# Kernel tuning notes

Measured on AMD Instinct MI355X. Metric: run time of the kernel, lower is better.

## Reference

```python
import jax, jax.numpy as jnp
import numpy as np

Lx = 32
Ly = 32
L = Lx * Ly          # 1024 lattice sites
N_E = L              # occupied orbitals (half filling of 2L BdG states)
HOPPING_LIST = (0, 2)
SWAVE_LIST = (0,)
DWAVE_LIST = (0,)


def _circulant_from_flat(flat, pad_front):
    """Faithful vectorized form of unroll_vpot_Mat: vmat[i,j] = V((xj-xi)%Lx,(yj-yi)%Ly)."""
    zero = jnp.zeros((1,), flat.dtype)
    v = jnp.concatenate([zero, flat, zero]) if pad_front else jnp.concatenate([flat, zero])
    A = v.reshape(1 + Lx // 2, 1 + Ly // 2)
    comp = jnp.block([[A, jnp.fliplr(A[:, 1:-1])],
                      [jnp.flipud(A[1:-1, :]), jnp.flipud(jnp.fliplr(A[1:-1, 1:-1]))]])  # (Lx,Ly)
    idx = jnp.arange(L)
    xs, ys = idx // Ly, idx % Ly
    DX = (xs[None, :] - xs[:, None]) % Lx
    DY = (ys[None, :] - ys[:, None]) % Ly
    return comp[DX, DY]  # (L, L)


def _fill_NN(X, nbr_a, nbr_b, sign):
    """Vectorized fill_NN_X/Y_matrix: scatter (X[j]-X[i])*sign[i,j] at (i, j=nbr)."""
    i = jnp.arange(L)
    M = jnp.zeros((L, L), X.dtype)
    M = M.at[i, nbr_a].set((X[nbr_a] - X[i]) * sign[i, nbr_a])
    M = M.at[i, nbr_b].set((X[nbr_b] - X[i]) * sign[i, nbr_b])
    return M


def setup_inputs() -> dict:
    rng = np.random.default_rng(0)
    key = jax.random.key(0)
    ks = jax.random.split(key, 16)

    # periodic square-lattice neighbor table: dirs 0:+y 1:+x 2:-y 3:-x
    idx = np.arange(L)
    x, y = idx // Ly, idx % Ly
    ivic = np.stack([
        x * Ly + (y + 1) % Ly,
        ((x + 1) % Lx) * Ly + y,
        x * Ly + (y - 1) % Ly,
        ((x - 1) % Lx) * Ly + y,
    ], axis=1)[:, :, None].astype(np.int32)  # (L,4,1)

    sign_b = (2.0 * rng.integers(0, 2, size=(L, L)) - 1.0).astype(np.float32)
    stagg = ((-1.0) ** (x + y)).astype(np.float32)

    def sym(k, n_mat):
        R = jax.random.normal(k, (n_mat, 2 * L, 2 * L), dtype=jnp.float32) * 0.05
        return 0.5 * (R + jnp.swapaxes(R, -1, -2))

    nJ = (1 + Lx // 2) * (1 + Ly // 2) - 1  # 288
    occupied = rng.permutation(2 * L)[:N_E].astype(np.int32)

    return {
        "occupied_sites": jnp.asarray(occupied),
        "xloc": jnp.asarray(rng.integers(0, 2 * L, size=(L,)).astype(np.int32)),
        "S_z": jnp.asarray((2.0 * rng.integers(0, 2, size=(L,)) - 1.0).astype(np.float32)),
        "X_Phonons": jax.random.normal(ks[0], (L,), dtype=jnp.float32) * 0.1,
        "Y_Phonons": jax.random.normal(ks[1], (L,), dtype=jnp.float32) * 0.1,
        "hopping_values": jnp.full((len(HOPPING_LIST),), -1.0, dtype=jnp.float32),
        "sWave_pair_values": jnp.full((len(SWAVE_LIST),), 0.1, dtype=jnp.float32),
        "dWave_pair_values": jnp.full((len(DWAVE_LIST),), 0.1, dtype=jnp.float32),
        "Jastrow_spin": jax.random.normal(ks[2], (nJ,), dtype=jnp.float32) * 0.01,
        "Jastrow_coupling_Xel": jax.random.normal(ks[3], (nJ - 1,), dtype=jnp.float32) * 0.01,
        "Jastrow_coupling_Yel": jax.random.normal(ks[4], (nJ - 1,), dtype=jnp.float32) * 0.01,
        "phonons_XX_jastrow": jax.random.normal(ks[5], (nJ,), dtype=jnp.float32) * 0.01,
        "phonons_XY_jastrow": jax.random.normal(ks[6], (nJ,), dtype=jnp.float32) * 0.01,
        "phonons_YY_jastrow": jax.random.normal(ks[7], (nJ,), dtype=jnp.float32) * 0.01,
        "g": jnp.array([0.7], dtype=jnp.float32),
        "f_Swave": jnp.array([0.05], dtype=jnp.float32),
        "f_dwave": jnp.array([0.05], dtype=jnp.float32),
        "z_x": jnp.array([0.5], dtype=jnp.float32),
        "z_y": jnp.array([0.5], dtype=jnp.float32),
        "x_rescaled": jnp.array([0.3], dtype=jnp.float32),
        "y_rescaled": jnp.array([0.3], dtype=jnp.float32),
        "hopping_array_matrices": sym(ks[8], 3),
        "sWave_pair_array_matrices": sym(ks[9], 1),
        "dWave_pair_array_matrices": sym(ks[10], 1),
        "ivic": jnp.asarray(ivic),
        "bond_hopping_difference_sign": jnp.asarray(sign_b),
        "stagg_x": jnp.asarray(stagg),
        "stagg_y": jnp.asarray(stagg),
    }


def reference(occupied_sites, xloc, S_z, X_Phonons, Y_Phonons,
              hopping_values, sWave_pair_values, dWave_pair_values,
              Jastrow_spin, Jastrow_coupling_Xel, Jastrow_coupling_Yel,
              phonons_XX_jastrow, phonons_XY_jastrow, phonons_YY_jastrow,
              g, f_Swave, f_dwave, z_x, z_y, x_rescaled, y_rescaled,
              hopping_array_matrices, sWave_pair_array_matrices, dWave_pair_array_matrices,
              ivic, bond_hopping_difference_sign, stagg_x, stagg_y):
    sign_b = bond_hopping_difference_sign

    H0 = -1.0 * hopping_array_matrices[1]
    H0 = H0 + jnp.einsum('i,ijk->jk', hopping_values, hopping_array_matrices[jnp.array(HOPPING_LIST)])
    H0 = H0 + jnp.einsum('i,ijk->jk', sWave_pair_values, sWave_pair_array_matrices[jnp.array(SWAVE_LIST)])
    H0 = H0 + jnp.einsum('i,ijk->jk', dWave_pair_values, dWave_pair_array_matrices[jnp.array(DWAVE_LIST)])

    phonX = _fill_NN(X_Phonons, ivic[:, 1, 0], ivic[:, 3, 0], sign_b)
    phonY = _fill_NN(Y_Phonons, ivic[:, 0, 0], ivic[:, 2, 0], sign_b)
    P = phonX + phonY
    M = phonX - phonY
    Z = jnp.zeros((L, L), H0.dtype)
    H0 = H0 + g[0] * jnp.block([[P, Z], [Z, -P]])
    H0 = H0 + f_Swave[0] * jnp.block([[Z, P], [P, Z]])
    H0 = H0 + f_dwave[0] * jnp.block([[Z, M], [M, Z]])

    eigs, U = jnp.linalg.eigh(H0)
    sgn, logdet = jnp.linalg.slogdet(U[occupied_sites, :N_E])

    vmat = _circulant_from_flat(Jastrow_spin, pad_front=False)
    log_jastrow = S_z @ vmat @ S_z

    coh = -0.5 * x_rescaled[0] * jnp.sum((X_Phonons - z_x * stagg_x) ** 2)
    coh = coh - 0.5 * y_rescaled[0] * jnp.sum((Y_Phonons - z_y * stagg_y) ** 2)
    vXX = _circulant_from_flat(phonons_XX_jastrow, pad_front=False)
    vXY = _circulant_from_flat(phonons_XY_jastrow, pad_front=False)
    vYY = _circulant_from_flat(phonons_YY_jastrow, pad_front=False)
    coh = coh + X_Phonons @ vXX @ X_Phonons
    coh = coh + Y_Phonons @ vXY @ X_Phonons + X_Phonons @ vXY @ Y_Phonons
    coh = coh + Y_Phonons @ vYY @ Y_Phonons

    # el-phonon jastrows: vmat * (X[i]-X[j]) * sign[i,j]
    vXel = _circulant_from_flat(Jastrow_coupling_Xel, pad_front=True) \
        * (X_Phonons[:, None] - X_Phonons[None, :]) * sign_b
    vYel = _circulant_from_flat(Jastrow_coupling_Yel, pad_front=True) \
        * (Y_Phonons[:, None] - Y_Phonons[None, :]) * sign_b
    coh = coh + S_z @ vXel @ S_z + S_z @ vYel @ S_z

    return logdet + coh + log_jastrow
```

## Files before the change

### kernel.cpp

```cpp
#include <hip/hip_runtime.h>
#include <math.h>

#define NN 2048
#define LL 1024
#define NSWB 5
#define NROUNDS (NSWB * 63)
#define PITER 10
#define JTAU 1e-6f
#define STREAK_FULL 2016


typedef float vf4 __attribute__((ext_vector_type(4)));

__global__ void build_H(const float* __restrict__ hop,  const float* __restrict__ swm,
                        const float* __restrict__ dwm,  const float* __restrict__ hv,
                        const float* __restrict__ sv,   const float* __restrict__ dv,
                        const float* __restrict__ X,    const float* __restrict__ Y,
                        const int*   __restrict__ ivic, const float* __restrict__ sb,
                        const float* __restrict__ gg,   const float* __restrict__ fS,
                        const float* __restrict__ fd,   float* __restrict__ W)
{
    int idx = blockIdx.x * 256 + threadIdx.x;
    int r = idx >> 11, c = idx & (NN - 1);
    float hv0 = hv[0], hv1 = hv[1], sv0 = sv[0], dv0 = dv[0];
    float g0 = gg[0], fS0 = fS[0], fd0 = fd[0];

    float val = 0.f;
    #pragma unroll
    for (int t = 0; t < 2; ++t) {
        int rr = t ? c : r;
        int cc = t ? r : c;
        int e  = rr * NN + cc;
        float v = hv0 * hop[e] - hop[NN*NN + e] + hv1 * hop[2*NN*NN + e]
                + sv0 * swm[e] + dv0 * dwm[e];
        int i = rr & (LL - 1), j = cc & (LL - 1);
        float px = 0.f, py = 0.f;
        float s = sb[i * LL + j];
        int n0 = ivic[i*4+0], n1 = ivic[i*4+1], n2 = ivic[i*4+2], n3 = ivic[i*4+3];
        if (j == n1 || j == n3) px = (X[j] - X[i]) * s;
        if (j == n0 || j == n2) py = (Y[j] - Y[i]) * s;
        float P = px + py, Mm = px - py;
        bool rlo = rr < LL, clo = cc < LL;
        if (rlo && clo)        v += g0 * P;
        else if (!rlo && !clo) v -= g0 * P;
        else                   v += fS0 * P + fd0 * Mm;
        val += 0.5f * v;
    }
    W[idx] = val;
}

__global__ void powv_init(float* v)
{
    int i = blockIdx.x * 256 + threadIdx.x;
    if (i < NN) {
        unsigned h = (unsigned)i * 2654435761u;
        h ^= h >> 13; h *= 2246822519u; h ^= h >> 16;
        v[i] = ((h >> 8) * (1.0f / 16777216.f)) - 0.5f;
    }
}

__global__ void matvec(const float* __restrict__ W, const float* __restrict__ vin,
                       float* __restrict__ vout, double* accslot)
{
    __shared__ float red[256];
    int row = blockIdx.x, tid = threadIdx.x;
    const float* wr = W + (size_t)row * NN;
    float s = 0.f;
    for (int j = tid; j < NN; j += 256) s += wr[j] * vin[j];
    red[tid] = s; __syncthreads();
    for (int off = 128; off; off >>= 1) { if (tid < off) red[tid] += red[tid + off]; __syncthreads(); }
    if (tid == 0) { float y = red[0]; vout[row] = y; atomicAdd(accslot, (double)y * (double)y); }
}

__global__ void add_shift(float* W, const double* acc)
{
    int i = blockIdx.x * 256 + threadIdx.x;
    if (i < NN) {
        double n1 = acc[8 + PITER - 1], n0 = acc[8 + PITER - 2];
        float rho = (float)sqrt(n1 / (n0 > 0.0 ? n0 : 1.0));
        W[(size_t)i * NN + i] += 1.45f * rho;
    }
}

__device__ __forceinline__ void pair_groups(int pair, int r, int& gp, int& gq)
{
    if (pair == 0) gp = 0;
    else { int t1 = pair - 1 + r; if (t1 >= 63) t1 -= 63; gp = 1 + t1; }
    int t2 = 62 - pair + r; if (t2 >= 63) t2 -= 63; gq = 1 + t2;
}

__device__ __forceinline__ int  ald(const int* p)
{ return __hip_atomic_load(p, __ATOMIC_RELAXED, __HIP_MEMORY_SCOPE_AGENT); }
__device__ __forceinline__ void ast(int* p, int v)
{ __hip_atomic_store(p, v, __ATOMIC_RELAXED, __HIP_MEMORY_SCOPE_AGENT); }
__device__ __forceinline__ void afst(float* p, float v)
{ __hip_atomic_store(p, v, __ATOMIC_RELAXED, __HIP_MEMORY_SCOPE_AGENT); }
__device__ __forceinline__ void afadd(float* p, float v)
{ (void)__hip_atomic_fetch_add(p, v, __ATOMIC_RELAXED, __HIP_MEMORY_SCOPE_AGENT); }

__device__ __forceinline__ vf4 cld4(const float* p)
{ vf4 d; asm volatile("global_load_dwordx4 %0, %1, off sc0 sc1" : "=v"(d) : "v"(p)); return d; }
__device__ __forceinline__ void cst4(float* p, vf4 v)
{ asm volatile("global_store_dwordx4 %0, %1, off sc0 sc1" :: "v"(p), "v"(v) : "memory"); }
__device__ __forceinline__ void cst1(float* p, float v)
{ asm volatile("global_store_dword %0, %1, off sc0 sc1" :: "v"(p), "v"(v) : "memory"); }
__device__ __forceinline__ void waitvm0()
{ asm volatile("s_waitcnt vmcnt(0)" ::: "memory"); __builtin_amdgcn_sched_barrier(0); }

__device__ __forceinline__ void gridbar(int* bars, int phase)
{
    waitvm0();
    __syncthreads();
    if (threadIdx.x == 0) {
        int g = blockIdx.x & 7;
        int old = __hip_atomic_fetch_add(&bars[g * 1024], 1,
                      __ATOMIC_RELAXED, __HIP_MEMORY_SCOPE_AGENT);
        if (old == phase * 64 - 1) {
            int t = __hip_atomic_fetch_add(&bars[8 * 1024], 1,
                        __ATOMIC_RELAXED, __HIP_MEMORY_SCOPE_AGENT);
            if (t == phase * 8 - 1)
                ast(&bars[9 * 1024], phase);
        }
        while (ald(&bars[9 * 1024]) < phase)
            __builtin_amdgcn_s_sleep(8);
        asm volatile("" ::: "memory");
    }
    __syncthreads();
}

__global__ __launch_bounds__(512, 4) void jac_fused(float* __restrict__ W,
                                                    float* __restrict__ Sg,
                                                    float* __restrict__ Vbuf,
                                                    int* __restrict__ gctl,
                                                    int* __restrict__ bars,
                                                    int* __restrict__ pbars,
                                                    int* __restrict__ vstat)
{
    __shared__ float TT[64][132];
    __shared__ float S[64][65];
    __shared__ float Vs[64][64];
    __shared__ float csC[32], csS[32];
    __shared__ int   pk[32], qk[32];
    __shared__ int   active;
    __shared__ int   nact[2];

    const int tid    = threadIdx.x;
    const int bid    = blockIdx.x;
    const int gpair  = bid >> 4, chunk = bid & 15;
    const int r0     = chunk * 128;
    const bool issol = (chunk == (gpair >> 1));
    const bool ldr   = (issol && tid == 0);
    int gphase = 0, pphase = 0;

    for (int rr = 0; rr < NROUNDS; ++rr) {
        int r = rr; while (r >= 63) r -= 63;
        int gp, gq; pair_groups(gpair, r, gp, gq);
        int c1 = ald(&gctl[2 + gp]);
        int c2 = ald(&gctl[2 + gq]);
        bool hint = (c1 >= 63 && c2 >= 63);
        if (!hint) ++pphase;

        {
            float* bufn = Sg + ((size_t)(((rr + 1) & 1) * 32 + gpair)) * 4096 + chunk * 256;
            if (tid < 256) afst(&bufn[tid], 0.f);
        }

        if (!hint) {
            {
                int q  = tid & 31, r4 = q << 2;
                int cA = tid >> 5;
                vf4 t0 = cld4(W + (size_t)(gp * 32 + cA     ) * NN + r0 + r4);
                vf4 t1 = cld4(W + (size_t)(gp * 32 + cA + 16) * NN + r0 + r4);
                vf4 t2 = cld4(W + (size_t)(gq * 32 + cA     ) * NN + r0 + r4);
                vf4 t3 = cld4(W + (size_t)(gq * 32 + cA + 16) * NN + r0 + r4);
                waitvm0();
                *(vf4*)&TT[cA     ][r4] = t0;
                *(vf4*)&TT[cA + 16][r4] = t1;
                *(vf4*)&TT[cA + 32][r4] = t2;
                *(vf4*)&TT[cA + 48][r4] = t3;
            }
            __syncthreads();
            int tr = tid & 15, tc = tid >> 4;
            float acc[4][2] = {};
            for (int r4 = 0; r4 < 128; r4 += 4) {
                float a[4][4], b[2][4];
                #pragma unroll
                for (int m = 0; m < 4; ++m) *(float4*)a[m] = *(const float4*)&TT[tr + 16*m][r4];
                #pragma unroll
                for (int n = 0; n < 2; ++n) *(float4*)b[n] = *(const float4*)&TT[tc + 32*n][r4];
                #pragma unroll
                for (int m = 0; m < 4; ++m)
                    #pragma unroll
                    for (int n = 0; n < 2; ++n)
                        #pragma unroll
                        for (int k = 0; k < 4; ++k)
                            acc[m][n] += a[m][k] * b[n][k];
            }
            float* bufc = Sg + ((size_t)((rr & 1) * 32 + gpair)) * 4096;
            #pragma unroll
            for (int m = 0; m < 4; ++m)
                #pragma unroll
                for (int n = 0; n < 2; ++n)
                    afadd(&bufc[(tr + 16*m) * 64 + (tc + 32*n)], acc[m][n]);
            waitvm0();
            __syncthreads();
            if (tid == 0)
                (void)__hip_atomic_fetch_add(&pbars[gpair * 1024], 1,
                          __ATOMIC_RELAXED, __HIP_MEMORY_SCOPE_AGENT);
        }

        int do_apply = 0;
        if (hint) {
            if (ldr) {
                ast(&gctl[2 + gp], c1 + 1);
                ast(&gctl[2 + gq], c2 + 1);
                int old = __hip_atomic_fetch_add(&gctl[1], 1,
                              __ATOMIC_RELAXED, __HIP_MEMORY_SCOPE_AGENT);
                if (old + 1 >= STREAK_FULL) ast(&gctl[0], 1);
            }
        } else if (issol) {
            if (tid == 0) {
                while (ald(&pbars[gpair * 1024]) < 16 * pphase)
                    __builtin_amdgcn_s_sleep(4);
                active = 0;
            }
            if (tid < 2) nact[tid] = 0;
            __syncthreads();
            {
                const float* bufc = Sg + ((size_t)((rr & 1) * 32 + gpair)) * 4096;
                vf4 s0 = cld4(bufc + 4 * tid);
                vf4 s1 = cld4(bufc + 4 * (tid + 512));
                waitvm0();
                int i0 = tid >> 4, j0 = (tid & 15) << 2;
                int i1 = (tid + 512) >> 4;
                S[i0][j0] = s0.x; S[i0][j0+1] = s0.y; S[i0][j0+2] = s0.z; S[i0][j0+3] = s0.w;
                S[i1][j0] = s1.x; S[i1][j0+1] = s1.y; S[i1][j0+2] = s1.z; S[i1][j0+3] = s1.w;
            }
            __syncthreads();
            int loc = 0;
            for (int e = tid; e < 4096; e += 512) {
                int i = e >> 6, j = e & 63;
                if (i < j) {
                    float o = S[i][j];
                    if (o * o > JTAU * S[i][i] * S[j][j]) loc = 1;
                }
            }
            if (loc) active = 1;
            __syncthreads();
            if (!active) {
                if (tid == 0) {
                    ast(&gctl[2 + gp], c1 + 1);
                    ast(&gctl[2 + gq], c2 + 1);
                    int old = __hip_atomic_fetch_add(&gctl[1], 1,
                                  __ATOMIC_RELAXED, __HIP_MEMORY_SCOPE_AGENT);
                    if (old + 1 >= STREAK_FULL) ast(&gctl[0], 1);
                    ast(&vstat[gpair * 32], pphase * 2);
                }
            } else {
                do_apply = 1;
                if (tid == 0) {
                    ast(&gctl[2 + gp], 0);
                    ast(&gctl[2 + gq], 0);
                    __hip_atomic_exchange(&gctl[1], 0,
                        __ATOMIC_RELAXED, __HIP_MEMORY_SCOPE_AGENT);
                }
                int lane = tid & 63, wv = tid >> 6;
                float v[8];
                #pragma unroll
                for (int i = 0; i < 8; ++i) v[i] = (8 * wv + i == lane) ? 1.f : 0.f;

                for (int r2 = 0; r2 < 63; ++r2) {
                    if (tid < 32) {
                        int k = tid, p, q;
                        if (k == 0) p = 0;
                        else { int t1 = k - 1 + r2; if (t1 >= 63) t1 -= 63; p = 1 + t1; }
                        int t2 = 62 - k + r2; if (t2 >= 63) t2 -= 63; q = 1 + t2;
                        float app = S[p][p], aqq = S[q][q], apq = S[p][q];
                        float c = 1.f, s = 0.f;
                        if (apq * apq > JTAU * app * aqq) {
                            float tau = (aqq - app) * __builtin_amdgcn_rcpf(2.f * apq);
                            float sq  = __builtin_amdgcn_sqrtf(fmaf(tau, tau, 1.f));
                            float t   = (tau >= 0.f ? 1.f : -1.f) *
                                        __builtin_amdgcn_rcpf(fabsf(tau) + sq);
                            c = __builtin_amdgcn_rsqf(fmaf(t, t, 1.f));
                            s = t * c;
                            nact[r2 & 1] = 1;
                        }
                        csC[k] = c; csS[k] = s; pk[k] = p; qk[k] = q;
                    }
                    if (tid == 256) nact[(r2 + 1) & 1] = 0;
                    __syncthreads();
                    if (!nact[r2 & 1]) break;
                    for (int u = tid; u < 1024; u += 512) {
                        int ki = u >> 5, kj = u & 31;
                        float si_ = csS[ki], sj_ = csS[kj];
                        if (si_ == 0.f && sj_ == 0.f) continue;
                        float ci_ = csC[ki], cj_ = csC[kj];
                        int pi = pk[ki], qi = qk[ki], pj = pk[kj], qj = qk[kj];
                        float a  = S[pi][pj], b  = S[pi][qj];
                        float c2 = S[qi][pj], d  = S[qi][qj];
                        float a1 = cj_ * a  - sj_ * b,  b1 = sj_ * a  + cj_ * b;
                        float c1 = cj_ * c2 - sj_ * d,  d1 = sj_ * c2 + cj_ * d;
                        S[pi][pj] = ci_ * a1 - si_ * c1;
                        S[qi][pj] = si_ * a1 + ci_ * c1;
                        S[pi][qj] = ci_ * b1 - si_ * d1;
                        S[qi][qj] = si_ * b1 + ci_ * d1;
                    }
                    {
                        int k;
                        if (lane == 0) k = 0;
                        else { int t = lane - 1 - r2; if (t < 0) t += 63;
                               k = (t <= 30) ? (t + 1) : (62 - t); }
                        float s_ = csS[k];
                        if (s_ != 0.f) {
                            float c_ = csC[k];
                            int p = pk[k], q = qk[k];
                            bool isp = (lane == p);
                            int part = isp ? q : p;
                            #pragma unroll
                            for (int i = 0; i < 8; ++i) {
                                float other = __shfl(v[i], part);
                                v[i] = isp ? (c_ * v[i] - s_ * other)
                                           : (s_ * other + c_ * v[i]);
                            }
                        }
                    }
                    __syncthreads();
                }
                float* vb = Vbuf + ((size_t)gpair << 12);
                #pragma unroll
                for (int i = 0; i < 8; ++i) {
                    Vs[8 * wv + i][lane] = v[i];
                    cst1(vb + (8 * wv + i) * 64 + lane, v[i]);
                }
                waitvm0();
                __syncthreads();
                if (tid == 0) ast(&vstat[gpair * 32], pphase * 2 + 1);
            }
        } else {
            if (tid == 0) {
                int v;
                while ((v = ald(&vstat[gpair * 32])) < pphase * 2)
                    __builtin_amdgcn_s_sleep(4);
                active = v & 1;
                asm volatile("" ::: "memory");
            }
            __syncthreads();
            if (active) {
                do_apply = 1;
                const float* vb = Vbuf + ((size_t)gpair << 12);
                vf4 a0 = cld4(vb + 4 * tid);
                vf4 a1 = cld4(vb + 4 * (tid + 512));
                waitvm0();
                int i0 = tid >> 4, j0 = (tid & 15) << 2;
                int i1 = (tid + 512) >> 4;
                *(vf4*)&Vs[i0][j0] = a0;
                *(vf4*)&Vs[i1][j0] = a1;
                __syncthreads();
            }
        }

        if (do_apply) {
            int rt = tid & 31, ct = tid >> 5;
            int rr0 = rt << 2, c20 = ct << 2;
            float acc[4][4] = {};
            for (int c = 0; c < 64; ++c) {
                float a[4], b[4];
                *(float4*)a = *(const float4*)&TT[c][rr0];
                *(float4*)b = *(const float4*)&Vs[c][c20];
                #pragma unroll
                for (int i = 0; i < 4; ++i)
                    #pragma unroll
                    for (int j = 0; j < 4; ++j)
                        acc[i][j] += a[i] * b[j];
            }
            __syncthreads();
            #pragma unroll
            for (int j = 0; j < 4; ++j)
                #pragma unroll
                for (int i = 0; i < 4; ++i)
                    TT[c20 + j][rr0 + i] = acc[i][j];
            __syncthreads();
            {
                int q  = tid & 31, r4 = q << 2;
                int cA = tid >> 5;
                cst4(W + (size_t)(gp * 32 + cA     ) * NN + r0 + r4, *(const vf4*)&TT[cA     ][r4]);
                cst4(W + (size_t)(gp * 32 + cA + 16) * NN + r0 + r4, *(const vf4*)&TT[cA + 16][r4]);
                cst4(W + (size_t)(gq * 32 + cA     ) * NN + r0 + r4, *(const vf4*)&TT[cA + 32][r4]);
                cst4(W + (size_t)(gq * 32 + cA + 16) * NN + r0 + r4, *(const vf4*)&TT[cA + 48][r4]);
            }
        }
        gridbar(bars, ++gphase);
        if (ald(&gctl[0])) break;
    }
}

__global__ void colnorms(const float* __restrict__ W, float* __restrict__ sig2)
{
    __shared__ float red[256];
    int col = blockIdx.x, tid = threadIdx.x;
    const float* c = W + (size_t)col * NN;
    float s = 0.f;
    for (int e = tid; e < NN; e += 256) s += c[e] * c[e];
    red[tid] = s; __syncthreads();
    for (int off = 128; off; off >>= 1) { if (tid < off) red[tid] += red[tid + off]; __syncthreads(); }
    if (tid == 0) sig2[col] = red[0];
}

__global__ void select_k(const float* __restrict__ sig2, int* __restrict__ sel)
{
    int i = blockIdx.x * 256 + threadIdx.x;
    if (i >= NN) return;
    float di = sig2[i]; int rank = 0;
    for (int j = 0; j < NN; ++j) {
        float dj = sig2[j];
        rank += (dj < di) || (dj == di && j < i);
    }
    if (rank < LL) sel[rank] = i;
}

__global__ void gather_M(const float* __restrict__ W, const float* __restrict__ sig2,
                         const int* __restrict__ sel, const int* __restrict__ occ,
                         float* __restrict__ Mt)
{
    int idx = blockIdx.x * 256 + threadIdx.x;
    int b = idx >> 10, a = idx & (LL - 1);
    int col = sel[b];
    float rn = 1.f / sqrtf(sig2[col]);
    Mt[(size_t)b * LL + a] = W[(size_t)col * NN + occ[a]] * rn;
}

__global__ void gram(const float* __restrict__ Mt, double* __restrict__ G)
{
    __shared__ float As[32][17], Bs[32][17];
    int t = threadIdx.x;
    int tx = t & 15, ty = t >> 4;
    int a0 = blockIdx.y * 16, c0 = blockIdx.x * 16;
    double s = 0.0;
    for (int kb = 0; kb < LL; kb += 32) {
        for (int u = t; u < 32 * 16; u += 256) {
            int kr = u >> 4, i = u & 15;
            As[kr][i] = Mt[(size_t)(kb + kr) * LL + a0 + i];
            Bs[kr][i] = Mt[(size_t)(kb + kr) * LL + c0 + i];
        }
        __syncthreads();
        #pragma unroll 8
        for (int k2 = 0; k2 < 32; ++k2)
            s += (double)As[k2][ty] * (double)Bs[k2][tx];
        __syncthreads();
    }
    G[(size_t)(a0 + ty) * LL + (c0 + tx)] = s;
}

__global__ void chol_panel(double* __restrict__ G, int k0, double* __restrict__ acc)
{
    __shared__ double Ld[64][65];
    __shared__ double sinv;
    int tid = threadIdx.x;
    for (int u = tid; u < 4096; u += 256)
        Ld[u >> 6][u & 63] = G[(size_t)(k0 + (u >> 6)) * LL + k0 + (u & 63)];
    __syncthreads();
    double lsum = 0.0;
    for (int c = 0; c < 64; ++c) {
        if (tid == 0) {
            double d = Ld[c][c]; d = d > 1e-300 ? d : 1e-300;
            double sd = sqrt(d); lsum += log(sd);
            Ld[c][c] = sd; sinv = 1.0 / sd;
        }
        __syncthreads();
        if (tid < 63 - c) Ld[c + 1 + tid][c] *= sinv;
        __syncthreads();
        for (int u = tid; u < 4096; u += 256) {
            int rr = u >> 6, cc = u & 63;
            if (rr > c && cc > c) Ld[rr][cc] -= Ld[rr][c] * Ld[cc][c];
        }
        __syncthreads();
    }
    for (int u = tid; u < 4096; u += 256)
        G[(size_t)(k0 + (u >> 6)) * LL + k0 + (u & 63)] = Ld[u >> 6][u & 63];
    if (tid == 0) atomicAdd(acc + 1, lsum);
}

__global__ void chol_trsm(double* __restrict__ G, int k0)
{
    __shared__ double L11[64][65];
    __shared__ double Rt[32][65];
    int tid = threadIdx.x;
    int rbase = k0 + 64 + blockIdx.x * 32;
    for (int u = tid; u < 4096; u += 256)
        L11[u >> 6][u & 63] = G[(size_t)(k0 + (u >> 6)) * LL + k0 + (u & 63)];
    for (int u = tid; u < 2048; u += 256)
        Rt[u >> 6][u & 63] = G[(size_t)(rbase + (u >> 6)) * LL + k0 + (u & 63)];
    __syncthreads();
    for (int c = 0; c < 64; ++c) {
        if (tid < 32) Rt[tid][c] *= 1.0 / L11[c][c];
        __syncthreads();
        for (int u = tid; u < 2048; u += 256) {
            int rr = u >> 6, cc = u & 63;
            if (cc > c) Rt[rr][cc] -= Rt[rr][c] * L11[cc][c];
        }
        __syncthreads();
    }
    for (int u = tid; u < 2048; u += 256)
        G[(size_t)(rbase + (u >> 6)) * LL + k0 + (u & 63)] = Rt[u >> 6][u & 63];
}

__global__ void chol_syrk(double* __restrict__ G, int k0)
{
    __shared__ double At[64][32];
    __shared__ double Bt[64][32];
    int tid = threadIdx.x;
    int r0g = k0 + 64 + blockIdx.y * 64;
    int c0g = k0 + 64 + blockIdx.x * 64;
    int i0 = (tid >> 4) << 2, j0 = (tid & 15) << 2;
    double acc[4][4] = {};
    for (int kh = 0; kh < 2; ++kh) {
        for (int u = tid; u < 2048; u += 256) {
            int i = u >> 5, c = u & 31;
            At[i][c] = G[(size_t)(r0g + i) * LL + k0 + kh * 32 + c];
            Bt[i][c] = G[(size_t)(c0g + i) * LL + k0 + kh * 32 + c];
        }
        __syncthreads();
        for (int c = 0; c < 32; ++c) {
            int cr = (c + tid) & 31;
            double a[4], b[4];
            #pragma unroll
            for (int i = 0; i < 4; ++i) a[i] = At[i0 + i][cr];
            #pragma unroll
            for (int j = 0; j < 4; ++j) b[j] = Bt[j0 + j][cr];
            #pragma unroll
            for (int i = 0; i < 4; ++i)
                #pragma unroll
                for (int j = 0; j < 4; ++j)
                    acc[i][j] += a[i] * b[j];
        }
        __syncthreads();
    }
    #pragma unroll
    for (int i = 0; i < 4; ++i)
        #pragma unroll
        for (int j = 0; j < 4; ++j) {
            size_t e = (size_t)(r0g + i0 + i) * LL + c0g + j0 + j;
            G[e] -= acc[i][j];
        }
}

__global__ void pair_sums(const float* __restrict__ Sz,  const float* __restrict__ X,
                          const float* __restrict__ Y,
                          const float* __restrict__ Jsp, const float* __restrict__ JXel,
                          const float* __restrict__ JYel,const float* __restrict__ pXX,
                          const float* __restrict__ pXY, const float* __restrict__ pYY,
                          const float* __restrict__ sb,  const float* __restrict__ stx,
                          const float* __restrict__ sty,
                          const float* __restrict__ zx,  const float* __restrict__ zy,
                          const float* __restrict__ xr,  const float* __restrict__ yr,
                          double* __restrict__ acc)
{
    __shared__ float tS[289], tXe[289], tYe[289], tXX[289], tXY[289], tYY[289];
    __shared__ double red[256];
    int tid = threadIdx.x;
    for (int u = tid; u < 289; u += 256) {
        tS[u]  = (u < 288) ? Jsp[u] : 0.f;
        tXX[u] = (u < 288) ? pXX[u] : 0.f;
        tXY[u] = (u < 288) ? pXY[u] : 0.f;
        tYY[u] = (u < 288) ? pYY[u] : 0.f;
        tXe[u] = (u >= 1 && u < 288) ? JXel[u - 1] : 0.f;
        tYe[u] = (u >= 1 && u < 288) ? JYel[u - 1] : 0.f;
    }
    __syncthreads();
    int idx = blockIdx.x * 256 + tid;
    int i = idx >> 10, j = idx & (LL - 1);
    int xi = i >> 5, yi = i & 31, xj = j >> 5, yj = j & 31;
    int dx = (xj - xi) & 31, dy = (yj - yi) & 31;
    int rx = (dx <= 16) ? dx : 32 - dx;
    int ry = (dy <= 16) ? dy : 32 - dy;
    int ti = rx * 17 + ry;
    float si = Sz[i], sj = Sz[j];
    float Xi = X[i], Xj = X[j], Yi = Y[i], Yj = Y[j];
    float sbij = sb[i * LL + j];
    double sum = (double)(si * sj) * (double)tS[ti];
    sum += (double)(Xi * Xj) * (double)tXX[ti];
    sum += (double)(Yi * Xj + Xi * Yj) * (double)tXY[ti];
    sum += (double)(Yi * Yj) * (double)tYY[ti];
    sum += (double)(si * sj * sbij) *
           ((double)tXe[ti] * (double)(Xi - Xj) + (double)tYe[ti] * (double)(Yi - Yj));
    if (i == j) {
        float ex = Xi - zx[0] * stx[i];
        float ey = Yi - zy[0] * sty[i];
        sum -= 0.5 * (double)xr[0] * ex * ex + 0.5 * (double)yr[0] * ey * ey;
    }
    red[tid] = sum; __syncthreads();
    for (int off = 128; off; off >>= 1) { if (tid < off) red[tid] += red[tid + off]; __syncthreads(); }
    if (tid == 0) atomicAdd(&acc[0], red[0]);
}

__global__ void finalize(const double* __restrict__ acc, float* __restrict__ out)
{
    out[0] = (float)(acc[0] + acc[1]);
}

extern "C" void kernel_launch(void* const* d_in, const int* in_sizes, int n_in,
                              void* d_out, int out_size, void* d_ws, size_t ws_size,
                              hipStream_t stream)
{
    const int*   occ  = (const int*)  d_in[0];
    const float* Sz   = (const float*)d_in[2];
    const float* X    = (const float*)d_in[3];
    const float* Y    = (const float*)d_in[4];
    const float* hv   = (const float*)d_in[5];
    const float* sv   = (const float*)d_in[6];
    const float* dv   = (const float*)d_in[7];
    const float* Jsp  = (const float*)d_in[8];
    const float* JXel = (const float*)d_in[9];
    const float* JYel = (const float*)d_in[10];
    const float* pXX  = (const float*)d_in[11];
    const float* pXY  = (const float*)d_in[12];
    const float* pYY  = (const float*)d_in[13];
    const float* g    = (const float*)d_in[14];
    const float* fS   = (const float*)d_in[15];
    const float* fd   = (const float*)d_in[16];
    const float* zx   = (const float*)d_in[17];
    const float* zy   = (const float*)d_in[18];
    const float* xr   = (const float*)d_in[19];
    const float* yr   = (const float*)d_in[20];
    const float* hop  = (const float*)d_in[21];
    const float* swm  = (const float*)d_in[22];
    const float* dwm  = (const float*)d_in[23];
    const int*   ivic = (const int*)  d_in[24];
    const float* sb   = (const float*)d_in[25];
    const float* stx  = (const float*)d_in[26];
    const float* sty  = (const float*)d_in[27];
    float* out = (float*)d_out;

    char* ws = (char*)d_ws;
    float*  W    = (float*) (ws + 0);
    float*  v0   = (float*) (ws + 16777216);
    float*  v1   = (float*) (ws + 16785408);
    float*  sig2 = (float*) (ws + 16793600);
    int*    sel  = (int*)   (ws + 16801792);
    float*  Mt   = (float*) (ws + 16805888);
    double* G    = (double*)(ws + 21000192);
    double* acc  = (double*)(ws + 29388800);
    int*    gctl = (int*)   (ws + 29389056);
    int*    bars  = (int*)  Mt;
    int*    pbars = bars + 10 * 1024;
    int*    vstat = pbars + 32 * 1024;
    float*  Vbuf  = (float*)(vstat + 1024);
    float*  Sg    = (float*)G;

    (void)hipMemsetAsync(acc, 0, 768, stream);
    (void)hipMemsetAsync(bars, 0, 44 * 4096, stream);
    (void)hipMemsetAsync(Sg, 0, 2 * 32 * 4096 * 4, stream);
    build_H<<<NN * NN / 256, 256, 0, stream>>>(hop, swm, dwm, hv, sv, dv, X, Y,
                                               ivic, sb, g, fS, fd, W);
    powv_init<<<8, 256, 0, stream>>>(v0);
    for (int it = 0; it < PITER; ++it) {
        const float* vin = (it & 1) ? v1 : v0;
        float* vout = (it & 1) ? v0 : v1;
        matvec<<<NN, 256, 0, stream>>>(W, vin, vout, acc + 8 + it);
    }
    add_shift<<<8, 256, 0, stream>>>(W, acc);

    jac_fused<<<512, 512, 0, stream>>>(W, Sg, Vbuf, gctl, bars, pbars, vstat);

    colnorms<<<NN, 256, 0, stream>>>(W, sig2);
    select_k<<<8, 256, 0, stream>>>(sig2, sel);
    gather_M<<<4096, 256, 0, stream>>>(W, sig2, sel, occ, Mt);
    gram<<<dim3(64, 64), 256, 0, stream>>>(Mt, G);

    for (int s = 0; s < 16; ++s) {
        int k0 = s * 64;
        chol_panel<<<1, 256, 0, stream>>>(G, k0, acc);
        int nrows = LL - k0 - 64;
        if (nrows > 0) {
            chol_trsm<<<nrows / 32, 256, 0, stream>>>(G, k0);
            chol_syrk<<<dim3(nrows / 64, nrows / 64), 256, 0, stream>>>(G, k0);
        }
    }

    pair_sums<<<4096, 256, 0, stream>>>(Sz, X, Y, Jsp, JXel, JYel, pXX, pXY, pYY,
                                        sb, stx, sty, zx, zy, xr, yr, acc);
    finalize<<<1, 1, 0, stream>>>(acc, out);
}
```

Baseline: 41.53 ms.

## Split inner Jacobi sweep into producer wave and consumer waves via LDS flags

The solver block's inner 64x64 Jacobi loop no longer has all 512 threads synchronise with __syncthreads every sweep step. Wave 0 alone computes the rotations and updates S, publishing each step's sines into an LDS history buffer and advancing a progress counter. Waves 1-4 spin on that counter and accumulate the eigenvector matrix with 16 rows each, recomputing cosine from sine. This removes block-wide barriers and lets the V accumulation overlap the S updates. The cost is that the S update now runs on one wave instead of eight. Recomputing c as sqrt(1-s^2) can also differ slightly in precision and loses any sign information carried by c.

```diff
diff --git a/kernel.cpp b/kernel.cpp
--- a/kernel.cpp
+++ b/kernel.cpp
@@ -89,6 +89,13 @@
     int t2 = 62 - pair + r; if (t2 >= 63) t2 -= 63; gq = 1 + t2;
 }
 
+__device__ __forceinline__ void rot_pq(int k, int r2, int& p, int& q)
+{
+    if (k == 0) p = 0;
+    else { int t1 = k - 1 + r2; if (t1 >= 63) t1 -= 63; p = 1 + t1; }
+    int t2 = 62 - k + r2; if (t2 >= 63) t2 -= 63; q = 1 + t2;
+}
+
 __device__ __forceinline__ int  ald(const int* p)
 { return __hip_atomic_load(p, __ATOMIC_RELAXED, __HIP_MEMORY_SCOPE_AGENT); }
 __device__ __forceinline__ void ast(int* p, int v)
@@ -106,6 +113,8 @@
 { asm volatile("global_store_dword %0, %1, off sc0 sc1" :: "v"(p), "v"(v) : "memory"); }
 __device__ __forceinline__ void waitvm0()
 { asm volatile("s_waitcnt vmcnt(0)" ::: "memory"); __builtin_amdgcn_sched_barrier(0); }
+__device__ __forceinline__ void waitlgkm0()
+{ asm volatile("s_waitcnt lgkmcnt(0)" ::: "memory"); __builtin_amdgcn_sched_barrier(0); }
 
 __device__ __forceinline__ void gridbar(int* bars, int phase)
 {
@@ -139,10 +148,10 @@
     __shared__ float TT[64][132];
     __shared__ float S[64][65];
     __shared__ float Vs[64][64];
+    __shared__ float sbuf[63 * 32];
     __shared__ float csC[32], csS[32];
-    __shared__ int   pk[32], qk[32];
+    __shared__ int   ibx[2];
     __shared__ int   active;
-    __shared__ int   nact[2];
 
     const int tid    = threadIdx.x;
     const int bid    = blockIdx.x;
@@ -150,6 +159,7 @@
     const int r0     = chunk * 128;
     const bool issol = (chunk == (gpair >> 1));
     const bool ldr   = (issol && tid == 0);
+    const int lane   = tid & 63, wv = tid >> 6;
     int gphase = 0, pphase = 0;
 
     for (int rr = 0; rr < NROUNDS; ++rr) {
@@ -224,7 +234,6 @@
                     __builtin_amdgcn_s_sleep(4);
                 active = 0;
             }
-            if (tid < 2) nact[tid] = 0;
             __syncthreads();
             {
                 const float* bufc = Sg + ((size_t)((rr & 1) * 32 + gpair)) * 4096;
@@ -263,18 +272,16 @@
                     ast(&gctl[2 + gq], 0);
                     __hip_atomic_exchange(&gctl[1], 0,
                         __ATOMIC_RELAXED, __HIP_MEMORY_SCOPE_AGENT);
+                    ibx[0] = 0;
+                    ibx[1] = 63;
                 }
-                int lane = tid & 63, wv = tid >> 6;
-                float v[8];
-                #pragma unroll
-                for (int i = 0; i < 8; ++i) v[i] = (8 * wv + i == lane) ? 1.f : 0.f;
-
-                for (int r2 = 0; r2 < 63; ++r2) {
-                    if (tid < 32) {
-                        int k = tid, p, q;
-                        if (k == 0) p = 0;
-                        else { int t1 = k - 1 + r2; if (t1 >= 63) t1 -= 63; p = 1 + t1; }
-                        int t2 = 62 - k + r2; if (t2 >= 63) t2 -= 63; q = 1 + t2;
+                __syncthreads();
+
+                if (wv == 0) {
+                    int r2final = 63;
+                    for (int r2 = 0; r2 < 63; ++r2) {
+                        int k = lane & 31;
+                        int p, q; rot_pq(k, r2, p, q);
                         float app = S[p][p], aqq = S[q][q], apq = S[p][q];
                         float c = 1.f, s = 0.f;
                         if (apq * apq > JTAU * app * aqq) {
@@ -284,56 +291,79 @@
                                         __builtin_amdgcn_rcpf(fabsf(tau) + sq);
                             c = __builtin_amdgcn_rsqf(fmaf(t, t, 1.f));
                             s = t * c;
-                            nact[r2 & 1] = 1;
                         }
-                        csC[k] = c; csS[k] = s; pk[k] = p; qk[k] = q;
+                        if (!__any(s != 0.f)) { r2final = r2; break; }
+                        if (lane < 32) {
+                            csC[k] = c; csS[k] = s;
+                            sbuf[r2 * 32 + k] = s;
+                        }
+                        waitlgkm0();
+                        if (lane == 0) *(volatile int*)&ibx[0] = r2 + 1;
+                        int ki = lane >> 1;
+                        int pi, qi; rot_pq(ki, r2, pi, qi);
+                        float cki = csC[ki], ski = csS[ki];
+                        int base = (lane & 1) << 4;
+                        #pragma unroll
+                        for (int j = 0; j < 16; ++j) {
+                            int kj = base + j;
+                            float ckj = csC[kj], skj = csS[kj];
+                            if (ski == 0.f && skj == 0.f) continue;
+                            int pj, qj; rot_pq(kj, r2, pj, qj);
+                            float a  = S[pi][pj], b  = S[pi][qj];
+                            float c2 = S[qi][pj], d  = S[qi][qj];
+                            float a1 = ckj * a  - skj * b,  b1 = skj * a  + ckj * b;
+                            float cc1 = ckj * c2 - skj * d, d1 = skj * c2 + ckj * d;
+                            S[pi][pj] = cki * a1 - ski * cc1;
+                            S[qi][pj] = ski * a1 + cki * cc1;
+                            S[pi][qj] = cki * b1 - ski * d1;
+                            S[qi][qj] = ski * b1 + cki * d1;
+                        }
                     }
-                    if (tid == 256) nact[(r2 + 1) & 1] = 0;
-                    __syncthreads();
-                    if (!nact[r2 & 1]) break;
-                    for (int u = tid; u < 1024; u += 512) {
-                        int ki = u >> 5, kj = u & 31;
-                        float si_ = csS[ki], sj_ = csS[kj];
-                        if (si_ == 0.f && sj_ == 0.f) continue;
-                        float ci_ = csC[ki], cj_ = csC[kj];
-                        int pi = pk[ki], qi = qk[ki], pj = pk[kj], qj = qk[kj];
-                        float a  = S[pi][pj], b  = S[pi][qj];
-                        float c2 = S[qi][pj], d  = S[qi][qj];
-                        float a1 = cj_ * a  - sj_ * b,  b1 = sj_ * a  + cj_ * b;
-                        float c1 = cj_ * c2 - sj_ * d,  d1 = sj_ * c2 + cj_ * d;
-                        S[pi][pj] = ci_ * a1 - si_ * c1;
-                        S[qi][pj] = si_ * a1 + ci_ * c1;
-                        S[pi][qj] = ci_ * b1 - si_ * d1;
-                        S[qi][qj] = si_ * b1 + ci_ * d1;
-                    }
-                    {
+                    if (lane == 0) *(volatile int*)&ibx[1] = r2final;
+                    waitlgkm0();
+                } else if (wv <= 4) {
+                    const int row0 = (wv - 1) << 4;
+                    float v[16];
+                    #pragma unroll
+                    for (int i = 0; i < 16; ++i) v[i] = (row0 + i == lane) ? 1.f : 0.f;
+                    int it = 0;
+                    while (true) {
+                        int done, total;
+                        while (true) {
+                            done  = *(volatile int*)&ibx[0];
+                            total = *(volatile int*)&ibx[1];
+                            if (done > it || total <= it) break;
+                            __builtin_amdgcn_s_sleep(1);
+                        }
+                        if (total <= it) break;
+                        waitlgkm0();
                         int k;
                         if (lane == 0) k = 0;
-                        else { int t = lane - 1 - r2; if (t < 0) t += 63;
+                        else { int t = lane - 1 - it; if (t < 0) t += 63;
                                k = (t <= 30) ? (t + 1) : (62 - t); }
-                        float s_ = csS[k];
+                        float s_ = sbuf[it * 32 + k];
                         if (s_ != 0.f) {
-                            float c_ = csC[k];
-                            int p = pk[k], q = qk[k];
+                            float c_ = __builtin_amdgcn_sqrtf(fmaf(-s_, s_, 1.f));
+                            int p, q; rot_pq(k, it, p, q);
                             bool isp = (lane == p);
                             int part = isp ? q : p;
                             #pragma unroll
-                            for (int i = 0; i < 8; ++i) {
+                            for (int i = 0; i < 16; ++i) {
                                 float other = __shfl(v[i], part);
                                 v[i] = isp ? (c_ * v[i] - s_ * other)
                                            : (s_ * other + c_ * v[i]);
                             }
                         }
+                        ++it;
                     }
-                    __syncthreads();
+                    float* vb = Vbuf + ((size_t)gpair << 12);
+                    #pragma unroll
+                    for (int i = 0; i < 16; ++i) {
+                        Vs[row0 + i][lane] = v[i];
+                        cst1(vb + (size_t)(row0 + i) * 64 + lane, v[i]);
+                    }
+                    waitvm0();
                 }
-                float* vb = Vbuf + ((size_t)gpair << 12);
-                #pragma unroll
-                for (int i = 0; i < 8; ++i) {
-                    Vs[8 * wv + i][lane] = v[i];
-                    cst1(vb + (8 * wv + i) * 64 + lane, v[i]);
-                }
-                waitvm0();
                 __syncthreads();
                 if (tid == 0) ast(&vstat[gpair * 32], pphase * 2 + 1);
             }
```

Measured after the change: 76.48 ms. +84.1%, slower.
